# Kernel tuning notes

Hardware: AMD Instinct MI355X
Metric: run time of the kernel (lower is better)

The kernel has to match this reference:

```python
import jax, jax.numpy as jnp
import numpy as np

B, S, H, NH, PF, L = 2, 2048, 1024, 16, 4096, 6
HD = H // NH
EPS = 1e-5


def setup_inputs() -> dict:
    key = jax.random.key(0)
    ks = jax.random.split(key, 12)
    s = lambda k, shp, fan: jax.random.normal(k, shp, jnp.float32) * (1.0 / np.sqrt(fan))
    return {
        "input_tensor": jax.random.normal(ks[0], (B, S, H), jnp.float32),
        "pos_emb": s(ks[1], (S, H), H),
        "Wq": s(ks[2], (L, H, H), H), "bq": jnp.zeros((L, H), jnp.float32),
        "Wk": s(ks[3], (L, H, H), H), "bk": jnp.zeros((L, H), jnp.float32),
        "Wv": s(ks[4], (L, H, H), H), "bv": jnp.zeros((L, H), jnp.float32),
        "Wo": s(ks[5], (L, H, H), H), "bo": jnp.zeros((L, H), jnp.float32),
        "ln_g": jnp.ones((L, H), jnp.float32), "ln_b": jnp.zeros((L, H), jnp.float32),
        "W1": s(ks[6], (L, H, PF), H), "b1": jnp.zeros((L, PF), jnp.float32),
        "W2": s(ks[7], (L, PF, H), PF), "b2": jnp.zeros((L, H), jnp.float32),
    }


def _layernorm(x, g, b):
    mu = jnp.mean(x, axis=-1, keepdims=True)
    var = jnp.mean(jnp.square(x - mu), axis=-1, keepdims=True)
    return (x - mu) * jax.lax.rsqrt(var + EPS) * g + b


def _encoder(input_tensor, pos_emb, params):
    # pos embed: same positions for every batch row
    src = input_tensor * jnp.sqrt(jnp.float32(H)) + pos_emb[None, :, :]

    def layer(src, p):
        Wq, bq, Wk, bk, Wv, bv, Wo, bo, g, b, W1, b1, W2, b2 = p
        q = (src @ Wq + bq).reshape(B, S, NH, HD)
        k = (src @ Wk + bk).reshape(B, S, NH, HD)
        v = (src @ Wv + bv).reshape(B, S, NH, HD)
        # scores [B, NH, S, S]
        energy = jnp.einsum("bqhd,bkhd->bhqk", q, k) / jnp.sqrt(jnp.float32(HD))
        attn = jax.nn.softmax(energy, axis=-1)
        ctx = jnp.einsum("bhqk,bkhd->bqhd", attn, v).reshape(B, S, H)
        attn_out = ctx @ Wo + bo
        src = _layernorm(src + attn_out, g, b)
        ffn = jax.nn.relu(src @ W1 + b1) @ W2 + b2
        src = _layernorm(src + ffn, g, b)  # same LayerNorm reused, as in source
        return src, None

    src, _ = jax.lax.scan(layer, src, params)
    return src


def reference(input_tensor, pos_emb, Wq, bq, Wk, bk, Wv, bv, Wo, bo, ln_g, ln_b, W1, b1, W2, b2):
    params = (Wq, bq, Wk, bk, Wv, bv, Wo, bo, ln_g, ln_b, W1, b1, W2, b2)
    return _encoder(input_tensor, pos_emb, params)
```

## Files before the change

### kernel.cpp

```cpp
#include <hip/hip_runtime.h>
#include <cstdint>

constexpr int Bc = 2, Sc = 2048, Hc = 1024, NHc = 16, HDc = 64, PFc = 4096, Lc = 6;
constexpr float EPSc = 1e-5f;
constexpr float QSC = 0.18033688011112042f;

using f32x4  = __attribute__((ext_vector_type(4))) float;
using bf16x8 = __attribute__((ext_vector_type(8))) __bf16;
using bf16x4 = __attribute__((ext_vector_type(4))) __bf16;
using u32x4  = __attribute__((ext_vector_type(4))) unsigned;

#if __has_builtin(__builtin_amdgcn_exp2f)
#define EXP2(x) __builtin_amdgcn_exp2f(x)
#else
#define EXP2(x) exp2f(x)
#endif

__device__ __forceinline__ f32x4 mfma16(bf16x8 a, bf16x8 b, f32x4 c) {
    return __builtin_amdgcn_mfma_f32_16x16x32_bf16(a, b, c, 0, 0, 0);
}

__device__ __forceinline__ void gload_lds16(const void* g, void* l) {
    __builtin_amdgcn_global_load_lds(
        (__attribute__((address_space(1))) void*)(uintptr_t)g,
        (__attribute__((address_space(3))) void*)(uint32_t)(uintptr_t)l,
        16, 0, 0);
}

template<int N> __device__ __forceinline__ void wait_vmcnt() {
    if constexpr (N == 0)      asm volatile("s_waitcnt vmcnt(0)" ::: "memory");
    else if constexpr (N == 6) asm volatile("s_waitcnt vmcnt(6)" ::: "memory");
    else if constexpr (N == 8) asm volatile("s_waitcnt vmcnt(8)" ::: "memory");
}
__device__ __forceinline__ void wait_lgkm0() {
    asm volatile("s_waitcnt lgkmcnt(0)" ::: "memory");
    __builtin_amdgcn_sched_barrier(0);
}

struct HL { __bf16 h, l; };
__device__ __forceinline__ HL split2(float v) {
    HL r;
    r.h = (__bf16)v;
    r.l = (__bf16)(v - (float)r.h);
    return r;
}

__device__ __forceinline__ unsigned bfbits(__bf16 x) {
    return (unsigned)__builtin_bit_cast(unsigned short, x);
}
__device__ __forceinline__ unsigned packbf(float a, float b) {
    return bfbits((__bf16)a) | (bfbits((__bf16)b) << 16);
}

__device__ __forceinline__ int xcd_swz(int bid, int nwg) {
    return (bid & 7) * (nwg >> 3) + (bid >> 3);
}

__global__ __launch_bounds__(256) void wconv_kernel(
    const float* __restrict__ in, __bf16* __restrict__ out, int K, int N)
{
    __shared__ float tile[64][65];
    const int t = threadIdx.x;
    const size_t lstride = (size_t)K * N;
    const float* ip = in + (size_t)blockIdx.z * lstride;
    __bf16* op = out + (size_t)blockIdx.z * lstride;
    const int n0 = blockIdx.x * 64, k0 = blockIdx.y * 64;
    #pragma unroll
    for (int c = 0; c < 4; ++c) {
        int idx = c * 256 + t;
        int row = idx >> 4;
        int c4  = idx & 15;
        float4 v = *(const float4*)(ip + (size_t)(k0 + row) * N + n0 + c4 * 4);
        tile[row][c4 * 4 + 0] = v.x; tile[row][c4 * 4 + 1] = v.y;
        tile[row][c4 * 4 + 2] = v.z; tile[row][c4 * 4 + 3] = v.w;
    }
    __syncthreads();
    #pragma unroll
    for (int c = 0; c < 4; ++c) {
        int idx = c * 256 + t;
        int n  = idx >> 4;
        int k4 = idx & 15;
        bf16x4 hh = { (__bf16)tile[k4 * 4 + 0][n], (__bf16)tile[k4 * 4 + 1][n],
                      (__bf16)tile[k4 * 4 + 2][n], (__bf16)tile[k4 * 4 + 3][n] };
        *(bf16x4*)(op + (size_t)(n0 + n) * K + k0 + k4 * 4) = hh;
    }
}

__global__ __launch_bounds__(256) void wconv2_kernel(
    const float* __restrict__ in, __bf16* __restrict__ outh,
    __bf16* __restrict__ outl, int K, int N)
{
    __shared__ float tile[64][65];
    const int t = threadIdx.x;
    const int n0 = blockIdx.x * 64, k0 = blockIdx.y * 64;
    #pragma unroll
    for (int c = 0; c < 4; ++c) {
        int idx = c * 256 + t;
        int row = idx >> 4;
        int c4  = idx & 15;
        float4 v = *(const float4*)(in + (size_t)(k0 + row) * N + n0 + c4 * 4);
        tile[row][c4 * 4 + 0] = v.x; tile[row][c4 * 4 + 1] = v.y;
        tile[row][c4 * 4 + 2] = v.z; tile[row][c4 * 4 + 3] = v.w;
    }
    __syncthreads();
    #pragma unroll
    for (int c = 0; c < 4; ++c) {
        int idx = c * 256 + t;
        int n  = idx >> 4;
        int k4 = idx & 15;
        HL e0 = split2(tile[k4 * 4 + 0][n]);
        HL e1 = split2(tile[k4 * 4 + 1][n]);
        HL e2 = split2(tile[k4 * 4 + 2][n]);
        HL e3 = split2(tile[k4 * 4 + 3][n]);
        bf16x4 hh = { e0.h, e1.h, e2.h, e3.h };
        bf16x4 ll = { e0.l, e1.l, e2.l, e3.l };
        *(bf16x4*)(outh + (size_t)(n0 + n) * K + k0 + k4 * 4) = hh;
        *(bf16x4*)(outl + (size_t)(n0 + n) * K + k0 + k4 * 4) = ll;
    }
}

__global__ __launch_bounds__(256) void embed_kernel(
    const float* __restrict__ in, const float* __restrict__ pos,
    float* __restrict__ sf, __bf16* __restrict__ sh, __bf16* __restrict__ sl)
{
    const int n4 = (Bc * Sc * Hc) / 4;
    const int pmask = (Sc * Hc / 4) - 1;
    for (int i = blockIdx.x * 256 + threadIdx.x; i < n4; i += gridDim.x * 256) {
        float4 a = ((const float4*)in)[i];
        float4 p = ((const float4*)pos)[i & pmask];
        float4 r;
        r.x = a.x * 32.f + p.x; r.y = a.y * 32.f + p.y;
        r.z = a.z * 32.f + p.z; r.w = a.w * 32.f + p.w;
        ((float4*)sf)[i] = r;
        HL e0 = split2(r.x), e1 = split2(r.y), e2 = split2(r.z), e3 = split2(r.w);
        bf16x4 hh = { e0.h, e1.h, e2.h, e3.h };
        bf16x4 ll = { e0.l, e1.l, e2.l, e3.l };
        ((bf16x4*)sh)[i] = hh;
        ((bf16x4*)sl)[i] = ll;
    }
}

template<int BM, int OUTMODE, bool RELU>
__global__ __launch_bounds__(256) void gemm_bt_kernel(
    const __bf16* __restrict__ A, const __bf16* __restrict__ Wt,
    const float* __restrict__ bias, void* __restrict__ out,
    int M, int N, int K)
{
    constexpr int MI = BM / 32;
    constexpr int LPT = BM / 32 + 4;
    __shared__ alignas(16) __bf16 Alds[2][BM * 64];
    __shared__ alignas(16) __bf16 Blds[2][128 * 64];

    const int tid = threadIdx.x, lane = tid & 63, wave = tid >> 6;
    const int lr = lane & 15, lg = lane >> 4;
    const int nbx = gridDim.x;
    const int swz = xcd_swz(blockIdx.y * nbx + blockIdx.x, nbx * gridDim.y);
    const int m0 = (swz / nbx) * BM, n0 = (swz % nbx) * 128;
    const int wm = (wave >> 1) * (BM / 2), wn = (wave & 1) * 64;

    f32x4 acc[MI][4] = {};

    auto stage = [&](int k0, int buf) {
        #pragma unroll
        for (int c = 0; c < BM / 32; ++c) {
            int li = c * 256 + tid;
            int row = li >> 3;
            int lcb = ((li & 7) << 4) ^ ((row & 7) << 4);
            gload_lds16(A + (size_t)(m0 + row) * K + k0 + (lcb >> 1),
                        (char*)Alds[buf] + (size_t)(c * 256 + wave * 64) * 16);
        }
        #pragma unroll
        for (int c = 0; c < 4; ++c) {
            int li = c * 256 + tid;
            int row = li >> 3;
            int lcb = ((li & 7) << 4) ^ ((row & 7) << 4);
            gload_lds16(Wt + (size_t)(n0 + row) * K + k0 + (lcb >> 1),
                        (char*)Blds[buf] + (size_t)(c * 256 + wave * 64) * 16);
        }
    };

    stage(0, 0);
    if (K > 64) stage(64, 1);

    for (int k0 = 0; k0 < K; k0 += 64) {
        const int cur = (k0 >> 6) & 1;
        if (k0 + 64 < K) wait_vmcnt<LPT>();
        else             wait_vmcnt<0>();
        __builtin_amdgcn_s_barrier();

        bf16x8 af[2][MI], bfr[2][4];
        #pragma unroll
        for (int ks = 0; ks < 2; ++ks) {
            #pragma unroll
            for (int i = 0; i < MI; ++i) {
                int ra = wm + i * 16 + lr;
                int pa = (ks * 64 + lg * 16) ^ ((ra & 7) << 4);
                af[ks][i] = *(const bf16x8*)((const char*)Alds[cur] + ra * 128 + pa);
            }
            #pragma unroll
            for (int i = 0; i < 4; ++i) {
                int rb = wn + i * 16 + lr;
                int pb = (ks * 64 + lg * 16) ^ ((rb & 7) << 4);
                bfr[ks][i] = *(const bf16x8*)((const char*)Blds[cur] + rb * 128 + pb);
            }
        }
        wait_lgkm0();
        __builtin_amdgcn_s_barrier();
        if (k0 + 128 < K) stage(k0 + 128, cur);

        __builtin_amdgcn_s_setprio(1);
        #pragma unroll
        for (int ks = 0; ks < 2; ++ks)
            #pragma unroll
            for (int mi = 0; mi < MI; ++mi)
                #pragma unroll
                for (int ni = 0; ni < 4; ++ni)
                    acc[mi][ni] = mfma16(af[ks][mi], bfr[ks][ni], acc[mi][ni]);
        __builtin_amdgcn_s_setprio(0);
    }

    #pragma unroll
    for (int ni = 0; ni < 4; ++ni) {
        int col = n0 + wn + ni * 16 + lr;
        float bv = bias[col];
        #pragma unroll
        for (int mi = 0; mi < MI; ++mi) {
            int rowb = m0 + wm + mi * 16 + lg * 4;
            #pragma unroll
            for (int r = 0; r < 4; ++r) {
                float v = acc[mi][ni][r] + bv;
                if (RELU) v = fmaxf(v, 0.f);
                size_t idx = (size_t)(rowb + r) * N + col;
                if constexpr (OUTMODE == 0) ((float*)out)[idx] = v;
                else                        ((__bf16*)out)[idx] = (__bf16)v;
            }
        }
    }
}

struct QKVBT {
    const __bf16 *wq, *wk, *wv;
    const float *bq, *bk, *bv;
    __bf16 *q, *k, *v;
};

__global__ __launch_bounds__(256) void qkv_bt_kernel(
    const __bf16* __restrict__ A, QKVBT a)
{
    constexpr int N = Hc, K = Hc;
    constexpr int LPT = 8;
    __shared__ alignas(16) __bf16 Alds[2][128 * 64];
    __shared__ alignas(16) __bf16 Blds[2][128 * 64];

    const int tid = threadIdx.x, lane = tid & 63, wave = tid >> 6;
    const int lr = lane & 15, lg = lane >> 4;
    const int nbx = gridDim.x;
    const int swz = xcd_swz(blockIdx.y * nbx + blockIdx.x, nbx * gridDim.y);
    const int gx = swz % nbx;
    const int widx = gx >> 3;
    const int n0 = (gx & 7) * 128;
    const int m0 = (swz / nbx) * 128;
    const int wm = (wave >> 1) * 64, wn = (wave & 1) * 64;

    const __bf16* Wt  = (widx == 0) ? a.wq : (widx == 1) ? a.wk : a.wv;
    const float* bias = (widx == 0) ? a.bq : (widx == 1) ? a.bk : a.bv;

    f32x4 acc[4][4] = {};

    auto stage = [&](int k0, int buf) {
        #pragma unroll
        for (int c = 0; c < 4; ++c) {
            int li = c * 256 + tid;
            int row = li >> 3;
            int lcb = ((li & 7) << 4) ^ ((row & 7) << 4);
            gload_lds16(A + (size_t)(m0 + row) * K + k0 + (lcb >> 1),
                        (char*)Alds[buf] + (size_t)(c * 256 + wave * 64) * 16);
            gload_lds16(Wt + (size_t)(n0 + row) * K + k0 + (lcb >> 1),
                        (char*)Blds[buf] + (size_t)(c * 256 + wave * 64) * 16);
        }
    };

    stage(0, 0);
    stage(64, 1);

    for (int k0 = 0; k0 < K; k0 += 64) {
        const int cur = (k0 >> 6) & 1;
        if (k0 + 64 < K) wait_vmcnt<LPT>();
        else             wait_vmcnt<0>();
        __builtin_amdgcn_s_barrier();

        bf16x8 af[2][4], bfr[2][4];
        #pragma unroll
        for (int ks = 0; ks < 2; ++ks) {
            #pragma unroll
            for (int i = 0; i < 4; ++i) {
                int ra = wm + i * 16 + lr;
                int pa = (ks * 64 + lg * 16) ^ ((ra & 7) << 4);
                af[ks][i] = *(const bf16x8*)((const char*)Alds[cur] + ra * 128 + pa);
                int rb = wn + i * 16 + lr;
                int pb = (ks * 64 + lg * 16) ^ ((rb & 7) << 4);
                bfr[ks][i] = *(const bf16x8*)((const char*)Blds[cur] + rb * 128 + pb);
            }
        }
        wait_lgkm0();
        __builtin_amdgcn_s_barrier();
        if (k0 + 128 < K) stage(k0 + 128, cur);

        __builtin_amdgcn_s_setprio(1);
        #pragma unroll
        for (int ks = 0; ks < 2; ++ks)
            #pragma unroll
            for (int mi = 0; mi < 4; ++mi)
                #pragma unroll
                for (int ni = 0; ni < 4; ++ni)
                    acc[mi][ni] = mfma16(af[ks][mi], bfr[ks][ni], acc[mi][ni]);
        __builtin_amdgcn_s_setprio(0);
    }

    __bf16* outp = (widx == 0) ? a.q : (widx == 1) ? a.k : a.v;
    const float osc = (widx == 0) ? QSC : 1.f;
    #pragma unroll
    for (int ni = 0; ni < 4; ++ni) {
        int col = n0 + wn + ni * 16 + lr;
        float bv = bias[col];
        int hh = col >> 6, d = col & 63;
        #pragma unroll
        for (int mi = 0; mi < 4; ++mi) {
            int rowb = m0 + wm + mi * 16 + lg * 4;
            #pragma unroll
            for (int r = 0; r < 4; ++r) {
                int row = rowb + r;
                int bb = row >> 11, s = row & (Sc - 1);
                outp[((size_t)(bb * NHc + hh) * Sc + s) * HDc + d] =
                    (__bf16)((acc[mi][ni][r] + bv) * osc);
            }
        }
    }
}

struct QKV0S {
    const __bf16 *wqh, *wql, *wkh, *wkl, *wv;
    const float *bq, *bk, *bv;
    __bf16 *qh, *ql, *kh, *kl, *vv;
};

__global__ __launch_bounds__(256) void qkv0s_kernel(
    const __bf16* __restrict__ Ahi, const __bf16* __restrict__ Alo, QKV0S a)
{
    constexpr int N = Hc, K = Hc;
    __shared__ alignas(16) __bf16 AldsH[128 * 64];
    __shared__ alignas(16) __bf16 AldsL[128 * 64];
    __shared__ alignas(16) __bf16 BldsH[128 * 64];
    __shared__ alignas(16) __bf16 BldsL[128 * 64];

    const int tid = threadIdx.x, lane = tid & 63, wave = tid >> 6;
    const int lr = lane & 15, lg = lane >> 4;
    const int nbx = gridDim.x;
    const int swz = xcd_swz(blockIdx.y * nbx + blockIdx.x, nbx * gridDim.y);
    const int gx = swz % nbx;
    const int widx = gx >> 3;
    const int n0 = (gx & 7) * 128;
    const int m0 = (swz / nbx) * 128;
    const int wm = (wave >> 1) * 64, wn = (wave & 1) * 64;
    const bool SPLIT = (widx < 2);

    const __bf16* Bh = (widx == 0) ? a.wqh : (widx == 1) ? a.wkh : a.wv;
    const __bf16* Bl = (widx == 0) ? a.wql : a.wkl;
    const float* bias = (widx == 0) ? a.bq : (widx == 1) ? a.bk : a.bv;

    f32x4 acc[4][4] = {};

    for (int k0 = 0; k0 < K; k0 += 64) {
        #pragma unroll
        for (int c = 0; c < 4; ++c) {
            int li = c * 256 + tid;
            int row = li >> 3;
            int lcb = ((li & 7) << 4) ^ ((row & 7) << 4);
            size_t aoff = (size_t)(m0 + row) * K + k0 + (lcb >> 1);
            size_t boff = (size_t)(n0 + row) * K + k0 + (lcb >> 1);
            size_t loff = (size_t)(c * 256 + wave * 64) * 16;
            gload_lds16(Ahi + aoff, (char*)AldsH + loff);
            gload_lds16(Bh + boff, (char*)BldsH + loff);
            if (SPLIT) {
                gload_lds16(Alo + aoff, (char*)AldsL + loff);
                gload_lds16(Bl + boff, (char*)BldsL + loff);
            }
        }
        __syncthreads();

        bf16x8 ah[2][4], al[2][4], bh[2][4], bl[2][4];
        #pragma unroll
        for (int ks = 0; ks < 2; ++ks) {
            #pragma unroll
            for (int i = 0; i < 4; ++i) {
                int ra = wm + i * 16 + lr;
                int pa = (ks * 64 + lg * 16) ^ ((ra & 7) << 4);
                ah[ks][i] = *(const bf16x8*)((const char*)AldsH + ra * 128 + pa);
                int rb = wn + i * 16 + lr;
                int pb = (ks * 64 + lg * 16) ^ ((rb & 7) << 4);
                bh[ks][i] = *(const bf16x8*)((const char*)BldsH + rb * 128 + pb);
                if (SPLIT) {
                    al[ks][i] = *(const bf16x8*)((const char*)AldsL + ra * 128 + pa);
                    bl[ks][i] = *(const bf16x8*)((const char*)BldsL + rb * 128 + pb);
                }
            }
        }
        #pragma unroll
        for (int ks = 0; ks < 2; ++ks)
            #pragma unroll
            for (int mi = 0; mi < 4; ++mi)
                #pragma unroll
                for (int ni = 0; ni < 4; ++ni) {
                    acc[mi][ni] = mfma16(ah[ks][mi], bh[ks][ni], acc[mi][ni]);
                    if (SPLIT) {
                        acc[mi][ni] = mfma16(al[ks][mi], bh[ks][ni], acc[mi][ni]);
                        acc[mi][ni] = mfma16(ah[ks][mi], bl[ks][ni], acc[mi][ni]);
                    }
                }
        __syncthreads();
    }

    __bf16* outh = (widx == 0) ? a.qh : (widx == 1) ? a.kh : a.vv;
    __bf16* outl = (widx == 0) ? a.ql : a.kl;
    const float osc = (widx == 0) ? QSC : 1.f;
    #pragma unroll
    for (int ni = 0; ni < 4; ++ni) {
        int col = n0 + wn + ni * 16 + lr;
        float bv = bias[col];
        int hh = col >> 6, d = col & 63;
        #pragma unroll
        for (int mi = 0; mi < 4; ++mi) {
            int rowb = m0 + wm + mi * 16 + lg * 4;
            #pragma unroll
            for (int r = 0; r < 4; ++r) {
                int row = rowb + r;
                int bb = row >> 11, s = row & (Sc - 1);
                size_t idx = ((size_t)(bb * NHc + hh) * Sc + s) * HDc + d;
                float v = (acc[mi][ni][r] + bv) * osc;
                if (SPLIT) {
                    HL e = split2(v);
                    outh[idx] = e.h;
                    outl[idx] = e.l;
                } else {
                    outh[idx] = (__bf16)v;
                }
            }
        }
    }
}

template<int QKSPLIT, int NH2>
__global__ __launch_bounds__(256) void attn_kernel(
    const __bf16* __restrict__ Qh, const __bf16* __restrict__ Ql,
    const __bf16* __restrict__ Kh, const __bf16* __restrict__ Kl,
    const __bf16* __restrict__ V, __bf16* __restrict__ O)
{
    constexpr int KVB = 64 * NH2;
    __shared__ alignas(16) __bf16 Ksh[2][KVB * 64];
    __shared__ alignas(16) __bf16 Klo[QKSPLIT ? 2 : 1][QKSPLIT ? 64 * 64 : 8];
    __shared__ alignas(16) __bf16 VT[2][NH2][64 * 64];

    const int tid = threadIdx.x;
    const int lane = tid & 63, wave = tid >> 6;
    const int lr = lane & 15, lg = lane >> 4;
    const int flat = blockIdx.x;
    const int hb = flat & 31;
    const int h = hb & 15, b = hb >> 4;
    const int q0 = (flat >> 5) * 128 + wave * 32;

    const size_t headoff = ((size_t)b * NHc + h) * Sc * HDc;
    const __bf16* Qb  = Qh + headoff;
    const __bf16* Kb  = Kh + headoff;
    const __bf16* Klb = QKSPLIT ? (Kl + headoff) : nullptr;
    const __bf16* Vb  = V + headoff;

    const size_t qrowA = (size_t)(q0 + lr) * HDc;
    const size_t qrowB = qrowA + 16 * HDc;
    bf16x8 qfA0 = *(const bf16x8*)(Qb + qrowA + lg * 8);
    bf16x8 qfA1 = *(const bf16x8*)(Qb + qrowA + 32 + lg * 8);
    bf16x8 qfB0 = *(const bf16x8*)(Qb + qrowB + lg * 8);
    bf16x8 qfB1 = *(const bf16x8*)(Qb + qrowB + 32 + lg * 8);
    bf16x8 qlA0, qlA1, qlB0, qlB1;
    if constexpr (QKSPLIT) {
        const __bf16* Qlb = Ql + headoff;
        qlA0 = *(const bf16x8*)(Qlb + qrowA + lg * 8);
        qlA1 = *(const bf16x8*)(Qlb + qrowA + 32 + lg * 8);
        qlB0 = *(const bf16x8*)(Qlb + qrowB + lg * 8);
        qlB1 = *(const bf16x8*)(Qlb + qrowB + 32 + lg * 8);
    }

    const int kp = tid & 31, dblk = tid >> 5;
    const int sp = (kp & 0x11) | ((kp & 0x06) << 1) | ((kp & 0x08) >> 2);

    auto stageK = [&](int kt, int buf) {
        #pragma unroll
        for (int c = 0; c < 2 * NH2; ++c) {
            int li  = c * 256 + tid;
            int row = li >> 3;
            int lcb = ((li & 7) << 4) ^ ((row & 7) << 4);
            size_t goff = (size_t)(kt * KVB + row) * HDc + (lcb >> 1);
            size_t loff = (size_t)(c * 256 + wave * 64) * 16;
            gload_lds16(Kb + goff, (char*)Ksh[buf] + loff);
            if constexpr (QKSPLIT)
                gload_lds16(Klb + goff, (char*)Klo[buf] + loff);
        }
    };
    auto loadV = [&](int kt, int half, bf16x8& va, bf16x8& vb2) {
        const __bf16* vs = Vb + (size_t)(kt * KVB + half * 64 + 2 * kp) * HDc + dblk * 8;
        va  = *(const bf16x8*)vs;
        vb2 = *(const bf16x8*)(vs + HDc);
    };
    auto writeVT = [&](int buf, int half, bf16x8 va, bf16x8 vb2) {
        #pragma unroll
        for (int j = 0; j < 8; ++j) {
            int d = dblk * 8 + j;
            unsigned u = bfbits(va[j]) | (bfbits(vb2[j]) << 16);
            int byte = d * 128 + ((sp * 4) ^ ((d & 7) << 4));
            *(unsigned*)((char*)VT[buf][half] + byte) = u;
        }
    };

    f32x4 oA[4] = {}, oB[4] = {};
    float mA = -1e30f, mB = -1e30f, lsA = 0.f, lsB = 0.f;

    stageK(0, 0);
    {
        bf16x8 va, vb2;
        #pragma unroll
        for (int hf = 0; hf < NH2; ++hf) {
            loadV(0, hf, va, vb2);
            writeVT(0, hf, va, vb2);
        }
    }
    __syncthreads();

    const int NT = Sc / KVB;
    int cur = 0;
    for (int kt = 0; kt < NT; ++kt) {
        const int nb = cur ^ 1;
        const bool pf = (kt + 1 < NT);
        bf16x8 va[NH2], vb2[NH2];
        if (pf) {
            stageK(kt + 1, nb);
            #pragma unroll
            for (int hf = 0; hf < NH2; ++hf) loadV(kt + 1, hf, va[hf], vb2[hf]);
        }

        const char* Kc  = (const char*)Ksh[cur];
        const char* Klc = (const char*)Klo[QKSPLIT ? cur : 0];

        #pragma unroll
        for (int half = 0; half < NH2; ++half) {
            f32x4 sA[4], sB[4];
            __builtin_amdgcn_s_setprio(1);
            #pragma unroll
            for (int kg = 0; kg < 4; ++kg) {
                int ra = half * 64 + kg * 16 + lr;
                int pa0 = (lg * 16) ^ ((ra & 7) << 4);
                int pa1 = (64 + lg * 16) ^ ((ra & 7) << 4);
                bf16x8 kf0 = *(const bf16x8*)(Kc + ra * 128 + pa0);
                bf16x8 kf1 = *(const bf16x8*)(Kc + ra * 128 + pa1);
                f32x4 tA = {}, tB = {};
                tA = mfma16(kf0, qfA0, tA);
                tA = mfma16(kf1, qfA1, tA);
                tB = mfma16(kf0, qfB0, tB);
                tB = mfma16(kf1, qfB1, tB);
                if constexpr (QKSPLIT) {
                    bf16x8 kg0 = *(const bf16x8*)(Klc + ra * 128 + pa0);
                    bf16x8 kg1 = *(const bf16x8*)(Klc + ra * 128 + pa1);
                    tA = mfma16(kg0, qfA0, tA);
                    tA = mfma16(kg1, qfA1, tA);
                    tA = mfma16(kf0, qlA0, tA);
                    tA = mfma16(kf1, qlA1, tA);
                    tB = mfma16(kg0, qfB0, tB);
                    tB = mfma16(kg1, qfB1, tB);
                    tB = mfma16(kf0, qlB0, tB);
                    tB = mfma16(kf1, qlB1, tB);
                }
                sA[kg] = tA;
                sB[kg] = tB;
            }
            __builtin_amdgcn_s_setprio(0);

            float mtA = -1e30f, mtB = -1e30f;
            #pragma unroll
            for (int kg = 0; kg < 4; ++kg)
                #pragma unroll
                for (int r = 0; r < 4; ++r) {
                    mtA = fmaxf(mtA, sA[kg][r]);
                    mtB = fmaxf(mtB, sB[kg][r]);
                }
            mtA = fmaxf(mtA, __shfl_xor(mtA, 16));
            mtA = fmaxf(mtA, __shfl_xor(mtA, 32));
            mtB = fmaxf(mtB, __shfl_xor(mtB, 16));
            mtB = fmaxf(mtB, __shfl_xor(mtB, 32));
            if (!__all(mtA <= mA + 8.f)) {
                float mnew = fmaxf(mA, mtA);
                float fac = EXP2(mA - mnew);
                mA = mnew;
                lsA *= fac;
                #pragma unroll
                for (int r = 0; r < 4; ++r) {
                    float fr = __shfl(fac, (lg << 4) | (lg * 4 + r));
                    #pragma unroll
                    for (int nd = 0; nd < 4; ++nd) oA[nd][r] *= fr;
                }
            }
            if (!__all(mtB <= mB + 8.f)) {
                float mnew = fmaxf(mB, mtB);
                float fac = EXP2(mB - mnew);
                mB = mnew;
                lsB *= fac;
                #pragma unroll
                for (int r = 0; r < 4; ++r) {
                    float fr = __shfl(fac, (lg << 4) | (lg * 4 + r));
                    #pragma unroll
                    for (int nd = 0; nd < 4; ++nd) oB[nd][r] *= fr;
                }
            }
            float psA = 0.f, psB = 0.f;
            #pragma unroll
            for (int kg = 0; kg < 4; ++kg)
                #pragma unroll
                for (int r = 0; r < 4; ++r) {
                    float pA = EXP2(sA[kg][r] - mA);
                    float pB = EXP2(sB[kg][r] - mB);
                    psA += pA;
                    psB += pB;
                    sA[kg][r] = pA;
                    sB[kg][r] = pB;
                }
            psA += __shfl_xor(psA, 16);
            psA += __shfl_xor(psA, 32);
            psB += __shfl_xor(psB, 16);
            psB += __shfl_xor(psB, 32);
            lsA += psA;
            lsB += psB;

            #pragma unroll
            for (int kh2 = 0; kh2 < 2; ++kh2) {
                u32x4 pkA, pkB;
                pkA[0] = packbf(sA[2 * kh2][0],     sA[2 * kh2][1]);
                pkA[1] = packbf(sA[2 * kh2][2],     sA[2 * kh2][3]);
                pkA[2] = packbf(sA[2 * kh2 + 1][0], sA[2 * kh2 + 1][1]);
                pkA[3] = packbf(sA[2 * kh2 + 1][2], sA[2 * kh2 + 1][3]);
                pkB[0] = packbf(sB[2 * kh2][0],     sB[2 * kh2][1]);
                pkB[1] = packbf(sB[2 * kh2][2],     sB[2 * kh2][3]);
                pkB[2] = packbf(sB[2 * kh2 + 1][0], sB[2 * kh2 + 1][1]);
                pkB[3] = packbf(sB[2 * kh2 + 1][2], sB[2 * kh2 + 1][3]);
                bf16x8 pafA = __builtin_bit_cast(bf16x8, pkA);
                bf16x8 pafB = __builtin_bit_cast(bf16x8, pkB);
                __builtin_amdgcn_s_setprio(1);
                #pragma unroll
                for (int nd = 0; nd < 4; ++nd) {
                    int d = nd * 16 + lr;
                    int byte = d * 128 + ((64 * kh2 + 16 * lg) ^ ((d & 7) << 4));
                    bf16x8 vbf = *(const bf16x8*)((const char*)VT[cur][half] + byte);
                    oA[nd] = mfma16(pafA, vbf, oA[nd]);
                    oB[nd] = mfma16(pafB, vbf, oB[nd]);
                }
                __builtin_amdgcn_s_setprio(0);
            }
        }

        if (pf) {
            #pragma unroll
            for (int hf = 0; hf < NH2; ++hf) writeVT(nb, hf, va[hf], vb2[hf]);
        }
        __syncthreads();
        cur = nb;
    }

    #pragma unroll
    for (int r = 0; r < 4; ++r) {
        float lvA = __shfl(lsA, (lg << 4) | (lg * 4 + r));
        float lvB = __shfl(lsB, (lg << 4) | (lg * 4 + r));
        float invA = 1.f / lvA;
        float invB = 1.f / lvB;
        size_t orowA = ((size_t)b * Sc + q0 + lg * 4 + r) * Hc + h * HDc;
        size_t orowB = orowA + (size_t)16 * Hc;
        #pragma unroll
        for (int nd = 0; nd < 4; ++nd) {
            O[orowA + nd * 16 + lr] = (__bf16)(oA[nd][r] * invA);
            O[orowB + nd * 16 + lr] = (__bf16)(oB[nd][r] * invB);
        }
    }
}

__global__ __launch_bounds__(256) void ln_kernel(
    const float* __restrict__ xr, const __bf16* __restrict__ y,
    const float* __restrict__ g, const float* __restrict__ beta,
    float* __restrict__ of, __bf16* __restrict__ oh)
{
    __shared__ float red[2][4];
    const int row = blockIdx.x, t = threadIdx.x;
    const int lane = t & 63, wave = t >> 6;
    const int idx = row * 256 + t;
    float4 a = ((const float4*)xr)[idx];
    bf16x4 cb = ((const bf16x4*)y)[idx];
    float4 v;
    v.x = a.x + (float)cb[0]; v.y = a.y + (float)cb[1];
    v.z = a.z + (float)cb[2]; v.w = a.w + (float)cb[3];
    float s1 = v.x + v.y + v.z + v.w;
    float s2 = v.x * v.x + v.y * v.y + v.z * v.z + v.w * v.w;
    #pragma unroll
    for (int off = 1; off < 64; off <<= 1) {
        s1 += __shfl_xor(s1, off);
        s2 += __shfl_xor(s2, off);
    }
    if (lane == 0) { red[0][wave] = s1; red[1][wave] = s2; }
    __syncthreads();
    s1 = red[0][0] + red[0][1] + red[0][2] + red[0][3];
    s2 = red[1][0] + red[1][1] + red[1][2] + red[1][3];
    const float mu   = s1 * (1.f / Hc);
    const float var  = s2 * (1.f / Hc) - mu * mu;
    const float rstd = rsqrtf(var + EPSc);
    float4 gg = ((const float4*)g)[t];
    float4 bb = ((const float4*)beta)[t];
    float4 r;
    r.x = (v.x - mu) * rstd * gg.x + bb.x;
    r.y = (v.y - mu) * rstd * gg.y + bb.y;
    r.z = (v.z - mu) * rstd * gg.z + bb.z;
    r.w = (v.w - mu) * rstd * gg.w + bb.w;
    ((float4*)of)[idx] = r;
    bf16x4 hh = { (__bf16)r.x, (__bf16)r.y, (__bf16)r.z, (__bf16)r.w };
    ((bf16x4*)oh)[idx] = hh;
}

extern "C" void kernel_launch(void* const* d_in, const int* in_sizes, int n_in,
                              void* d_out, int out_size, void* d_ws, size_t ws_size,
                              hipStream_t stream)
{
    const float* inp = (const float*)d_in[0];
    const float* pos = (const float*)d_in[1];
    const float* Wq  = (const float*)d_in[2];
    const float* bq  = (const float*)d_in[3];
    const float* Wk  = (const float*)d_in[4];
    const float* bk  = (const float*)d_in[5];
    const float* Wv  = (const float*)d_in[6];
    const float* bv  = (const float*)d_in[7];
    const float* Wo  = (const float*)d_in[8];
    const float* bo  = (const float*)d_in[9];
    const float* lng = (const float*)d_in[10];
    const float* lnb = (const float*)d_in[11];
    const float* W1  = (const float*)d_in[12];
    const float* b1  = (const float*)d_in[13];
    const float* W2  = (const float*)d_in[14];
    const float* b2  = (const float*)d_in[15];

    char* ws = (char*)d_ws;
    const size_t MB = 1u << 20;
    float*  src_f = (float*)(ws);
    __bf16* src_h = (__bf16*)(ws + 16 * MB);
    __bf16* src_l = (__bf16*)(ws + 24 * MB);
    __bf16* qh    = (__bf16*)(ws + 32 * MB);
    __bf16* kh    = (__bf16*)(ws + 40 * MB);
    __bf16* vv    = (__bf16*)(ws + 48 * MB);
    __bf16* ctx   = (__bf16*)(ws + 56 * MB);
    __bf16* ql    = (__bf16*)(ws + 64 * MB);
    __bf16* kl    = (__bf16*)(ws + 72 * MB);
    __bf16* tmpb  = (__bf16*)(ws + 80 * MB);
    __bf16* wq0h  = (__bf16*)(ws + 80 * MB);
    __bf16* wq0l  = (__bf16*)(ws + 82 * MB);
    __bf16* wk0h  = (__bf16*)(ws + 84 * MB);
    __bf16* wk0l  = (__bf16*)(ws + 86 * MB);
    __bf16* h1    = (__bf16*)(ws + 32 * MB);
    __bf16* wqT   = (__bf16*)(ws + 96 * MB);
    __bf16* wkT   = (__bf16*)(ws + 108 * MB);
    __bf16* wvT   = (__bf16*)(ws + 120 * MB);
    __bf16* woT   = (__bf16*)(ws + 132 * MB);
    __bf16* w1T   = (__bf16*)(ws + 144 * MB);
    __bf16* w2T   = (__bf16*)(ws + 192 * MB);

    const int M = Bc * Sc;

    wconv_kernel<<<dim3(16, 16, 6), 256, 0, stream>>>(Wq, wqT, Hc, Hc);
    wconv_kernel<<<dim3(16, 16, 6), 256, 0, stream>>>(Wk, wkT, Hc, Hc);
    wconv_kernel<<<dim3(16, 16, 6), 256, 0, stream>>>(Wv, wvT, Hc, Hc);
    wconv_kernel<<<dim3(16, 16, 6), 256, 0, stream>>>(Wo, woT, Hc, Hc);
    wconv_kernel<<<dim3(64, 16, 6), 256, 0, stream>>>(W1, w1T, Hc, PFc);
    wconv_kernel<<<dim3(16, 64, 6), 256, 0, stream>>>(W2, w2T, PFc, Hc);
    wconv2_kernel<<<dim3(16, 16), 256, 0, stream>>>(Wq, wq0h, wq0l, Hc, Hc);
    wconv2_kernel<<<dim3(16, 16), 256, 0, stream>>>(Wk, wk0h, wk0l, Hc, Hc);

    embed_kernel<<<2048, 256, 0, stream>>>(inp, pos, src_f, src_h, src_l);

    for (int l = 0; l < Lc; ++l) {
        const size_t wHH = (size_t)l * Hc * Hc;
        const size_t wH  = (size_t)l * Hc;
        if (l == 0) {
            QKV0S qa = { wq0h, wq0l, wk0h, wk0l, wvT, bq, bk, bv,
                         qh, ql, kh, kl, vv };
            qkv0s_kernel<<<dim3(24, 32), 256, 0, stream>>>(src_h, src_l, qa);
            attn_kernel<1, 1><<<512, 256, 0, stream>>>(qh, ql, kh, kl, vv, ctx);
        } else {
            QKVBT qa = { wqT + wHH, wkT + wHH, wvT + wHH, bq + wH, bk + wH, bv + wH,
                         qh, kh, vv };
            qkv_bt_kernel<<<dim3(24, 32), 256, 0, stream>>>(src_h, qa);
            attn_kernel<0, 2><<<512, 256, 0, stream>>>(qh, nullptr, kh, nullptr, vv, ctx);
        }
        gemm_bt_kernel<64, 1, false><<<dim3(8, 64), 256, 0, stream>>>(
            ctx, woT + wHH, bo + wH, tmpb, M, Hc, Hc);
        ln_kernel<<<M, 256, 0, stream>>>(src_f, tmpb, lng + wH, lnb + wH, src_f, src_h);
        gemm_bt_kernel<128, 1, true><<<dim3(32, 32), 256, 0, stream>>>(
            src_h, w1T + (size_t)l * Hc * PFc, b1 + (size_t)l * PFc, h1, M, PFc, Hc);
        gemm_bt_kernel<64, 1, false><<<dim3(8, 64), 256, 0, stream>>>(
            h1, w2T + (size_t)l * PFc * Hc, b2 + wH, tmpb, M, Hc, PFc);
        float* dst = (l == Lc - 1) ? (float*)d_out : src_f;
        ln_kernel<<<M, 256, 0, stream>>>(src_f, tmpb, lng + wH, lnb + wH, dst, src_h);
    }
}
```

Baseline: 1.508 ms.

## Shrink attention blocks to 16 query rows per wave and read K from global

The attention kernel now gives each wave one 16-row query tile instead of two, so each block covers 64 queries and the grid doubles to 1024 blocks. K is no longer staged into LDS via async global-to-LDS loads; each wave reads its K fragments directly from global memory. The launch bound now asks for 4 blocks per CU to raise occupancy with the smaller register and LDS footprint. The trade-off is that each K tile is fetched separately by every wave and re-read twice as often across blocks, relying on L1/L2 caching, and each K fragment now feeds half as many MFMAs.

```diff
diff --git a/kernel.cpp b/kernel.cpp
--- a/kernel.cpp
+++ b/kernel.cpp
@@ -450,14 +450,12 @@
 }
 
 template<int QKSPLIT, int NH2>
-__global__ __launch_bounds__(256) void attn_kernel(
+__global__ __launch_bounds__(256, 4) void attn_kernel(
     const __bf16* __restrict__ Qh, const __bf16* __restrict__ Ql,
     const __bf16* __restrict__ Kh, const __bf16* __restrict__ Kl,
     const __bf16* __restrict__ V, __bf16* __restrict__ O)
 {
     constexpr int KVB = 64 * NH2;
-    __shared__ alignas(16) __bf16 Ksh[2][KVB * 64];
-    __shared__ alignas(16) __bf16 Klo[QKSPLIT ? 2 : 1][QKSPLIT ? 64 * 64 : 8];
     __shared__ alignas(16) __bf16 VT[2][NH2][64 * 64];
 
     const int tid = threadIdx.x;
@@ -466,7 +464,7 @@
     const int flat = blockIdx.x;
     const int hb = flat & 31;
     const int h = hb & 15, b = hb >> 4;
-    const int q0 = (flat >> 5) * 128 + wave * 32;
+    const int q0 = (flat >> 5) * 64 + wave * 16;
 
     const size_t headoff = ((size_t)b * NHc + h) * Sc * HDc;
     const __bf16* Qb  = Qh + headoff;
@@ -474,37 +472,19 @@
     const __bf16* Klb = QKSPLIT ? (Kl + headoff) : nullptr;
     const __bf16* Vb  = V + headoff;
 
-    const size_t qrowA = (size_t)(q0 + lr) * HDc;
-    const size_t qrowB = qrowA + 16 * HDc;
-    bf16x8 qfA0 = *(const bf16x8*)(Qb + qrowA + lg * 8);
-    bf16x8 qfA1 = *(const bf16x8*)(Qb + qrowA + 32 + lg * 8);
-    bf16x8 qfB0 = *(const bf16x8*)(Qb + qrowB + lg * 8);
-    bf16x8 qfB1 = *(const bf16x8*)(Qb + qrowB + 32 + lg * 8);
-    bf16x8 qlA0, qlA1, qlB0, qlB1;
+    const size_t qrow = (size_t)(q0 + lr) * HDc;
+    bf16x8 qf0 = *(const bf16x8*)(Qb + qrow + lg * 8);
+    bf16x8 qf1 = *(const bf16x8*)(Qb + qrow + 32 + lg * 8);
+    bf16x8 qlo0, qlo1;
     if constexpr (QKSPLIT) {
         const __bf16* Qlb = Ql + headoff;
-        qlA0 = *(const bf16x8*)(Qlb + qrowA + lg * 8);
-        qlA1 = *(const bf16x8*)(Qlb + qrowA + 32 + lg * 8);
-        qlB0 = *(const bf16x8*)(Qlb + qrowB + lg * 8);
-        qlB1 = *(const bf16x8*)(Qlb + qrowB + 32 + lg * 8);
+        qlo0 = *(const bf16x8*)(Qlb + qrow + lg * 8);
+        qlo1 = *(const bf16x8*)(Qlb + qrow + 32 + lg * 8);
     }
 
     const int kp = tid & 31, dblk = tid >> 5;
     const int sp = (kp & 0x11) | ((kp & 0x06) << 1) | ((kp & 0x08) >> 2);
 
-    auto stageK = [&](int kt, int buf) {
-        #pragma unroll
-        for (int c = 0; c < 2 * NH2; ++c) {
-            int li  = c * 256 + tid;
-            int row = li >> 3;
-            int lcb = ((li & 7) << 4) ^ ((row & 7) << 4);
-            size_t goff = (size_t)(kt * KVB + row) * HDc + (lcb >> 1);
-            size_t loff = (size_t)(c * 256 + wave * 64) * 16;
-            gload_lds16(Kb + goff, (char*)Ksh[buf] + loff);
-            if constexpr (QKSPLIT)
-                gload_lds16(Klb + goff, (char*)Klo[buf] + loff);
-        }
-    };
     auto loadV = [&](int kt, int half, bf16x8& va, bf16x8& vb2) {
         const __bf16* vs = Vb + (size_t)(kt * KVB + half * 64 + 2 * kp) * HDc + dblk * 8;
         va  = *(const bf16x8*)vs;
@@ -520,10 +500,9 @@
         }
     };
 
-    f32x4 oA[4] = {}, oB[4] = {};
-    float mA = -1e30f, mB = -1e30f, lsA = 0.f, lsB = 0.f;
-
-    stageK(0, 0);
+    f32x4 o[4] = {};
+    float m = -1e30f, lsum = 0.f;
+
     {
         bf16x8 va, vb2;
         #pragma unroll
@@ -541,123 +520,82 @@
         const bool pf = (kt + 1 < NT);
         bf16x8 va[NH2], vb2[NH2];
         if (pf) {
-            stageK(kt + 1, nb);
             #pragma unroll
             for (int hf = 0; hf < NH2; ++hf) loadV(kt + 1, hf, va[hf], vb2[hf]);
         }
 
-        const char* Kc  = (const char*)Ksh[cur];
-        const char* Klc = (const char*)Klo[QKSPLIT ? cur : 0];
-
         #pragma unroll
         for (int half = 0; half < NH2; ++half) {
-            f32x4 sA[4], sB[4];
+            f32x4 s[4];
             __builtin_amdgcn_s_setprio(1);
             #pragma unroll
             for (int kg = 0; kg < 4; ++kg) {
-                int ra = half * 64 + kg * 16 + lr;
-                int pa0 = (lg * 16) ^ ((ra & 7) << 4);
-                int pa1 = (64 + lg * 16) ^ ((ra & 7) << 4);
-                bf16x8 kf0 = *(const bf16x8*)(Kc + ra * 128 + pa0);
-                bf16x8 kf1 = *(const bf16x8*)(Kc + ra * 128 + pa1);
-                f32x4 tA = {}, tB = {};
-                tA = mfma16(kf0, qfA0, tA);
-                tA = mfma16(kf1, qfA1, tA);
-                tB = mfma16(kf0, qfB0, tB);
-                tB = mfma16(kf1, qfB1, tB);
+                size_t krow = (size_t)(kt * KVB + half * 64 + kg * 16 + lr) * HDc;
+                bf16x8 kf0 = *(const bf16x8*)(Kb + krow + lg * 8);
+                bf16x8 kf1 = *(const bf16x8*)(Kb + krow + 32 + lg * 8);
+                f32x4 t = {};
+                t = mfma16(kf0, qf0, t);
+                t = mfma16(kf1, qf1, t);
                 if constexpr (QKSPLIT) {
-                    bf16x8 kg0 = *(const bf16x8*)(Klc + ra * 128 + pa0);
-                    bf16x8 kg1 = *(const bf16x8*)(Klc + ra * 128 + pa1);
-                    tA = mfma16(kg0, qfA0, tA);
-                    tA = mfma16(kg1, qfA1, tA);
-                    tA = mfma16(kf0, qlA0, tA);
-                    tA = mfma16(kf1, qlA1, tA);
-                    tB = mfma16(kg0, qfB0, tB);
-                    tB = mfma16(kg1, qfB1, tB);
-                    tB = mfma16(kf0, qlB0, tB);
-                    tB = mfma16(kf1, qlB1, tB);
+                    bf16x8 kl0 = *(const bf16x8*)(Klb + krow + lg * 8);
+                    bf16x8 kl1 = *(const bf16x8*)(Klb + krow + 32 + lg * 8);
+                    t = mfma16(kl0, qf0, t);
+                    t = mfma16(kl1, qf1, t);
+                    t = mfma16(kf0, qlo0, t);
+                    t = mfma16(kf1, qlo1, t);
                 }
-                sA[kg] = tA;
-                sB[kg] = tB;
+                s[kg] = t;
             }
             __builtin_amdgcn_s_setprio(0);
 
-            float mtA = -1e30f, mtB = -1e30f;
+            float mt = -1e30f;
             #pragma unroll
             for (int kg = 0; kg < 4; ++kg)
                 #pragma unroll
-                for (int r = 0; r < 4; ++r) {
-                    mtA = fmaxf(mtA, sA[kg][r]);
-                    mtB = fmaxf(mtB, sB[kg][r]);
-                }
-            mtA = fmaxf(mtA, __shfl_xor(mtA, 16));
-            mtA = fmaxf(mtA, __shfl_xor(mtA, 32));
-            mtB = fmaxf(mtB, __shfl_xor(mtB, 16));
-            mtB = fmaxf(mtB, __shfl_xor(mtB, 32));
-            if (!__all(mtA <= mA + 8.f)) {
-                float mnew = fmaxf(mA, mtA);
-                float fac = EXP2(mA - mnew);
-                mA = mnew;
-                lsA *= fac;
+                for (int r = 0; r < 4; ++r)
+                    mt = fmaxf(mt, s[kg][r]);
+            mt = fmaxf(mt, __shfl_xor(mt, 16));
+            mt = fmaxf(mt, __shfl_xor(mt, 32));
+            if (!__all(mt <= m + 8.f)) {
+                float mnew = fmaxf(m, mt);
+                float fac = EXP2(m - mnew);
+                m = mnew;
+                lsum *= fac;
                 #pragma unroll
                 for (int r = 0; r < 4; ++r) {
                     float fr = __shfl(fac, (lg << 4) | (lg * 4 + r));
                     #pragma unroll
-                    for (int nd = 0; nd < 4; ++nd) oA[nd][r] *= fr;
+                    for (int nd = 0; nd < 4; ++nd) o[nd][r] *= fr;
                 }
             }
-            if (!__all(mtB <= mB + 8.f)) {
-                float mnew = fmaxf(mB, mtB);
-                float fac = EXP2(mB - mnew);
-                mB = mnew;
-                lsB *= fac;
-                #pragma unroll
-                for (int r = 0; r < 4; ++r) {
-                    float fr = __shfl(fac, (lg << 4) | (lg * 4 + r));
-                    #pragma unroll
-                    for (int nd = 0; nd < 4; ++nd) oB[nd][r] *= fr;
-                }
-            }
-            float psA = 0.f, psB = 0.f;
+            float ps = 0.f;
             #pragma unroll
             for (int kg = 0; kg < 4; ++kg)
                 #pragma unroll
                 for (int r = 0; r < 4; ++r) {
-                    float pA = EXP2(sA[kg][r] - mA);
-                    float pB = EXP2(sB[kg][r] - mB);
-                    psA += pA;
-                    psB += pB;
-                    sA[kg][r] = pA;
-                    sB[kg][r] = pB;
+                    float p = EXP2(s[kg][r] - m);
+                    ps += p;
+                    s[kg][r] = p;
                 }
-            psA += __shfl_xor(psA, 16);
-            psA += __shfl_xor(psA, 32);
-            psB += __shfl_xor(psB, 16);
-            psB += __shfl_xor(psB, 32);
-            lsA += psA;
-            lsB += psB;
+            ps += __shfl_xor(ps, 16);
+            ps += __shfl_xor(ps, 32);
+            lsum += ps;
 
             #pragma unroll
             for (int kh2 = 0; kh2 < 2; ++kh2) {
-                u32x4 pkA, pkB;
-                pkA[0] = packbf(sA[2 * kh2][0],     sA[2 * kh2][1]);
-                pkA[1] = packbf(sA[2 * kh2][2],     sA[2 * kh2][3]);
-                pkA[2] = packbf(sA[2 * kh2 + 1][0], sA[2 * kh2 + 1][1]);
-                pkA[3] = packbf(sA[2 * kh2 + 1][2], sA[2 * kh2 + 1][3]);
-                pkB[0] = packbf(sB[2 * kh2][0],     sB[2 * kh2][1]);
-                pkB[1] = packbf(sB[2 * kh2][2],     sB[2 * kh2][3]);
-                pkB[2] = packbf(sB[2 * kh2 + 1][0], sB[2 * kh2 + 1][1]);
-                pkB[3] = packbf(sB[2 * kh2 + 1][2], sB[2 * kh2 + 1][3]);
-                bf16x8 pafA = __builtin_bit_cast(bf16x8, pkA);
-                bf16x8 pafB = __builtin_bit_cast(bf16x8, pkB);
+                u32x4 pk;
+                pk[0] = packbf(s[2 * kh2][0],     s[2 * kh2][1]);
+                pk[1] = packbf(s[2 * kh2][2],     s[2 * kh2][3]);
+                pk[2] = packbf(s[2 * kh2 + 1][0], s[2 * kh2 + 1][1]);
+                pk[3] = packbf(s[2 * kh2 + 1][2], s[2 * kh2 + 1][3]);
+                bf16x8 paf = __builtin_bit_cast(bf16x8, pk);
                 __builtin_amdgcn_s_setprio(1);
                 #pragma unroll
                 for (int nd = 0; nd < 4; ++nd) {
                     int d = nd * 16 + lr;
                     int byte = d * 128 + ((64 * kh2 + 16 * lg) ^ ((d & 7) << 4));
                     bf16x8 vbf = *(const bf16x8*)((const char*)VT[cur][half] + byte);
-                    oA[nd] = mfma16(pafA, vbf, oA[nd]);
-                    oB[nd] = mfma16(pafB, vbf, oB[nd]);
+                    o[nd] = mfma16(paf, vbf, o[nd]);
                 }
                 __builtin_amdgcn_s_setprio(0);
             }
@@ -673,17 +611,12 @@
 
     #pragma unroll
     for (int r = 0; r < 4; ++r) {
-        float lvA = __shfl(lsA, (lg << 4) | (lg * 4 + r));
-        float lvB = __shfl(lsB, (lg << 4) | (lg * 4 + r));
-        float invA = 1.f / lvA;
-        float invB = 1.f / lvB;
-        size_t orowA = ((size_t)b * Sc + q0 + lg * 4 + r) * Hc + h * HDc;
-        size_t orowB = orowA + (size_t)16 * Hc;
-        #pragma unroll
-        for (int nd = 0; nd < 4; ++nd) {
-            O[orowA + nd * 16 + lr] = (__bf16)(oA[nd][r] * invA);
-            O[orowB + nd * 16 + lr] = (__bf16)(oB[nd][r] * invB);
-        }
+        float lv  = __shfl(lsum, (lg << 4) | (lg * 4 + r));
+        float inv = 1.f / lv;
+        size_t orow = ((size_t)b * Sc + q0 + lg * 4 + r) * Hc + h * HDc;
+        #pragma unroll
+        for (int nd = 0; nd < 4; ++nd)
+            O[orow + nd * 16 + lr] = (__bf16)(o[nd][r] * inv);
     }
 }
 
@@ -792,12 +725,12 @@
             QKV0S qa = { wq0h, wq0l, wk0h, wk0l, wvT, bq, bk, bv,
                          qh, ql, kh, kl, vv };
             qkv0s_kernel<<<dim3(24, 32), 256, 0, stream>>>(src_h, src_l, qa);
-            attn_kernel<1, 1><<<512, 256, 0, stream>>>(qh, ql, kh, kl, vv, ctx);
+            attn_kernel<1, 1><<<1024, 256, 0, stream>>>(qh, ql, kh, kl, vv, ctx);
         } else {
             QKVBT qa = { wqT + wHH, wkT + wHH, wvT + wHH, bq + wH, bk + wH, bv + wH,
                          qh, kh, vv };
             qkv_bt_kernel<<<dim3(24, 32), 256, 0, stream>>>(src_h, qa);
-            attn_kernel<0, 2><<<512, 256, 0, stream>>>(qh, nullptr, kh, nullptr, vv, ctx);
+            attn_kernel<0, 2><<<1024, 256, 0, stream>>>(qh, nullptr, kh, nullptr, vv, ctx);
         }
         gemm_bt_kernel<64, 1, false><<<dim3(8, 64), 256, 0, stream>>>(
             ctx, woT + wHH, bo + wH, tmpb, M, Hc, Hc);
```

New measurement: 2.072 ms. 37.4% more time.
